# Kernel tuning notes

Measured on AMD Instinct MI355X. Metric: run time of the kernel, lower is better.

Reference implementation:

```python
import jax, jax.numpy as jnp
import numpy as np

B, S, E = 8, 2048, 1024
EPS = 1e-5

def _layernorm(x, w, b):
    mu = jnp.mean(x, axis=-1, keepdims=True)
    var = jnp.mean(jnp.square(x - mu), axis=-1, keepdims=True)
    return (x - mu) * jax.lax.rsqrt(var + EPS) * w + b

def setup_inputs() -> dict:
    key = jax.random.key(0)
    ks = jax.random.split(key, 12)
    x = jax.random.normal(ks[0], (B, S, E), dtype=jnp.float32)
    pad_mask = jax.random.randint(ks[1], (B, 1, S), 0, 2).astype(bool)
    pad_mask = pad_mask.at[:, :, 0].set(False)  # ensure no fully-masked row
    s = 1.0 / np.sqrt(E)
    Wq = jax.random.normal(ks[2], (E, E), jnp.float32) * s
    Wk = jax.random.normal(ks[3], (E, E), jnp.float32) * s
    Wv = jax.random.normal(ks[4], (E, E), jnp.float32) * s
    bq = jnp.zeros((E,), jnp.float32)
    bk = jnp.zeros((E,), jnp.float32)
    bv = jnp.zeros((E,), jnp.float32)
    W1 = jax.random.normal(ks[5], (2 * E, E), jnp.float32) * s
    b1 = jnp.zeros((2 * E,), jnp.float32)
    W2 = jax.random.normal(ks[6], (E, 2 * E), jnp.float32) * (1.0 / np.sqrt(2 * E))
    b2 = jnp.zeros((E,), jnp.float32)
    ln1_w = jnp.ones((E,), jnp.float32); ln1_b = jnp.zeros((E,), jnp.float32)
    ln2_w = jnp.ones((E,), jnp.float32); ln2_b = jnp.zeros((E,), jnp.float32)
    return {"x": x, "pad_mask": pad_mask, "ln1_w": ln1_w, "ln1_b": ln1_b,
            "ln2_w": ln2_w, "ln2_b": ln2_b, "Wq": Wq, "bq": bq, "Wk": Wk,
            "bk": bk, "Wv": Wv, "bv": bv, "W1": W1, "b1": b1, "W2": W2, "b2": b2}

def reference(x, pad_mask, ln1_w, ln1_b, ln2_w, ln2_b, Wq, bq, Wk, bk, Wv, bv, W1, b1, W2, b2):
    scale = jnp.sqrt(jnp.float32(x.shape[-1]))
    normed = _layernorm(x, ln1_w, ln1_b)
    Q = jnp.einsum('bse,de->bsd', normed, Wq) + bq
    K = jnp.einsum('bse,de->bsd', normed, Wk) + bk
    V = jnp.einsum('bse,de->bsd', normed, Wv) + bv
    scores = jnp.einsum('bqd,bkd->bqk', Q, K) / scale  # [B,S,S]
    scores = jnp.where(pad_mask, -jnp.inf, scores)
    attn = jax.nn.softmax(scores, axis=2)  # dropout is identity at inference
    x = x + jnp.einsum('bqk,bkd->bqd', attn, V)
    h = _layernorm(x, ln2_w, ln2_b)
    h = jax.nn.relu(jnp.einsum('bse,fe->bsf', h, W1) + b1)
    x = x + jnp.einsum('bsf,ef->bse', h, W2) + b2
    return x
```

## Files before the change

kernel.cpp:

```cpp
#include <hip/hip_runtime.h>
#include <hip/hip_bf16.h>
#include <cstdint>

#define B_ 8
#define S_ 2048
#define E_ 1024

using u16 = unsigned short;

typedef __bf16 bf16x8 __attribute__((ext_vector_type(8)));
typedef float f32x4 __attribute__((ext_vector_type(4)));

__device__ inline u16 f2bf(float f) {
  uint32_t u = __float_as_uint(f);
  uint32_t r = (u + 0x7fffu + ((u >> 16) & 1u)) >> 16;
  return (u16)r;
}

template<bool HAS_BIAS, bool RELU, bool HAS_RES, bool OUT_BF16, bool SCORES,
         bool GATHER_A, bool RUNTK>
__global__ __launch_bounds__(256, 2) void gemm_nt(
    const u16* __restrict__ A, const u16* __restrict__ B, void* __restrict__ C,
    const float* __restrict__ bias, const float* __restrict__ res,
    int lda, int ldb, int ldc, int K,
    long long strideA, long long strideB, long long strideC,
    const int* __restrict__ cidx, const int* __restrict__ cnt)
{
  __shared__ __attribute__((aligned(16))) u16 lA[2][128 * 64];
  __shared__ __attribute__((aligned(16))) u16 lB[2][128 * 64];

  const int tid  = threadIdx.x;
  const int lane = tid & 63;
  const int wave = tid >> 6;

  const int GM = 8, GN = 4;
  const int nbn = gridDim.x, nbm = gridDim.y, nz = gridDim.z;
  int bm, bn, bz;
  {
    const int total = nbn * nbm * nz;
    const long long lin = blockIdx.x +
        (long long)nbn * (blockIdx.y + (long long)nbm * blockIdx.z);
    if ((nbm % GM) == 0 && (nbn % GN) == 0 && (total % (8 * GM * GN)) == 0) {
      const int xcd = (int)(lin & 7);
      const int loc = (int)(lin >> 3);
      const int sper = GM * GN;
      const int super = (loc / sper) * 8 + xcd;
      const int ins   = loc % sper;
      const int spz = (nbm / GM) * (nbn / GN);
      bz = super / spz;
      const int s2 = super % spz;
      const int sm = s2 % (nbm / GM);
      const int sn = s2 / (nbm / GM);
      bm = sm * GM + (ins % GM);
      bn = sn * GN + (ins / GM);
    } else { bm = blockIdx.y; bn = blockIdx.x; bz = blockIdx.z; }
  }

  int count = 0, cpad = 0;
  if (SCORES || GATHER_A || RUNTK) {
    count = cnt[bz * 2];
    cpad  = cnt[bz * 2 + 1];
    if (GATHER_A && bm * 128 >= cpad) return;
    if (SCORES   && bn * 128 >= cpad) return;
  }
  const int Keff = RUNTK ? cpad : K;
  const int nk = Keff >> 6;

  const u16* Ab = A + (long long)bz * strideA;
  const u16* Bb = B + (long long)bz * strideB;

  const int srow = tid >> 3;
  const int scol = ((tid & 7) ^ (srow & 7)) * 8;
  long long rowA[4], rowB[4];
#pragma unroll
  for (int l = 0; l < 4; ++l) {
    int ra = bm * 128 + srow + l * 32;
    if (GATHER_A) ra = cidx[(long long)bz * S_ + ra];
    rowA[l] = (long long)ra * lda + scol;
    rowB[l] = (long long)(bn * 128 + srow + l * 32) * ldb + scol;
  }
  const int ldsoff = tid * 8;

  const int wr = wave >> 1, wc = wave & 1;
  const int rA = wr * 64 + (lane & 15);
  const int rB = wc * 64 + (lane & 15);
#define LDSP3(P) ((uint32_t)(uintptr_t)(__attribute__((address_space(3))) const void*)(P))
  uint32_t aA0 = LDSP3(&lA[0][0]) +
      2u * (uint32_t)(rA * 64 + (((0 * 4 + (lane >> 4)) ^ (rA & 7)) * 8));
  uint32_t aA1 = LDSP3(&lA[0][0]) +
      2u * (uint32_t)(rA * 64 + (((1 * 4 + (lane >> 4)) ^ (rA & 7)) * 8));
  uint32_t bB0 = LDSP3(&lB[0][0]) +
      2u * (uint32_t)(rB * 64 + (((0 * 4 + (lane >> 4)) ^ (rB & 7)) * 8));
  uint32_t bB1 = LDSP3(&lB[0][0]) +
      2u * (uint32_t)(rB * 64 + (((1 * 4 + (lane >> 4)) ^ (rB & 7)) * 8));
#undef LDSP3

  f32x4 acc[4][4];
#pragma unroll
  for (int mi = 0; mi < 4; ++mi)
#pragma unroll
    for (int ni = 0; ni < 4; ++ni)
      acc[mi][ni] = (f32x4){0.f, 0.f, 0.f, 0.f};

#define STAGE(T) {                                                             \
    const int tt_ = ((T) < nk) ? (T) : (nk - 1);                               \
    _Pragma("unroll") for (int l = 0; l < 4; ++l)                              \
      __builtin_amdgcn_global_load_lds(                                        \
          (const __attribute__((address_space(1))) void*)                      \
              (Ab + rowA[l] + (long long)tt_ * 64),                            \
          (__attribute__((address_space(3))) void*)                            \
              (&lA[(T) & 1][l * 2048 + ldsoff]),                               \
          16, 0, 0);                                                           \
    _Pragma("unroll") for (int l = 0; l < 4; ++l)                              \
      __builtin_amdgcn_global_load_lds(                                        \
          (const __attribute__((address_space(1))) void*)                      \
              (Bb + rowB[l] + (long long)tt_ * 64),                            \
          (__attribute__((address_space(3))) void*)                            \
              (&lB[(T) & 1][l * 2048 + ldsoff]),                               \
          16, 0, 0); }

#define DSR(D, ADDR, OFF) \
    asm volatile("ds_read_b128 %0, %1 offset:" OFF : "=v"(D) : "v"(ADDR))
#define LGKM(NSTR) asm volatile("s_waitcnt lgkmcnt(" NSTR ")" ::: "memory")
#define SCHED0()   __builtin_amdgcn_sched_barrier(0)
#define BAR()      __builtin_amdgcn_s_barrier()

#define MFMA_NI(NI) {                                                          \
    _Pragma("unroll") for (int mi = 0; mi < 4; ++mi)                           \
      _Pragma("unroll") for (int k2 = 0; k2 < 2; ++k2)                         \
        acc[mi][NI] = __builtin_amdgcn_mfma_f32_16x16x32_bf16(                 \
            af[mi][k2], bf[NI][k2], acc[mi][NI], 0, 0, 0); }

  STAGE(0);
  asm volatile("s_waitcnt vmcnt(0)" ::: "memory");
  BAR();

  bf16x8 af[4][2], bf[4][2];
  for (int t = 0; t < nk; ++t) {
    STAGE(t + 1);
    DSR(af[0][0], aA0, "0");     DSR(af[0][1], aA1, "0");
    DSR(af[1][0], aA0, "2048");  DSR(af[1][1], aA1, "2048");
    DSR(af[2][0], aA0, "4096");  DSR(af[2][1], aA1, "4096");
    DSR(af[3][0], aA0, "6144");  DSR(af[3][1], aA1, "6144");
    DSR(bf[0][0], bB0, "0");     DSR(bf[0][1], bB1, "0");
    DSR(bf[1][0], bB0, "2048");  DSR(bf[1][1], bB1, "2048");
    DSR(bf[2][0], bB0, "4096");  DSR(bf[2][1], bB1, "4096");
    DSR(bf[3][0], bB0, "6144");  DSR(bf[3][1], bB1, "6144");
    __builtin_amdgcn_s_setprio(1);
    LGKM("6"); SCHED0(); MFMA_NI(0);
    LGKM("4"); SCHED0(); MFMA_NI(1);
    LGKM("2"); SCHED0(); MFMA_NI(2);
    LGKM("0"); SCHED0(); MFMA_NI(3);
    __builtin_amdgcn_s_setprio(0);
    asm volatile("s_waitcnt vmcnt(0)" ::: "memory");
    BAR();
    const uint32_t d = (t & 1) ? (uint32_t)-16384 : 16384u;
    aA0 += d; aA1 += d; bB0 += d; bB1 += d;
  }

#undef MFMA_NI
#undef DSR
#undef STAGE
#undef BAR
#undef LGKM
#undef SCHED0

  const float* resb = (const float*)C;
  if (HAS_RES) resb = res + (long long)bz * strideC;
  u16*   cb16 = (u16*)C   + (long long)bz * strideC;
  float* cf32 = (float*)C + (long long)bz * strideC;

#pragma unroll
  for (int ni = 0; ni < 4; ++ni) {
    const int gn = bn * 128 + wc * 64 + ni * 16 + (lane & 15);
    const float bvv = HAS_BIAS ? bias[gn] : 0.f;
    const bool cmask = SCORES && (gn >= count);
#pragma unroll
    for (int mi = 0; mi < 4; ++mi) {
#pragma unroll
      for (int r = 0; r < 4; ++r) {
        const int gm = bm * 128 + wr * 64 + mi * 16 + (lane >> 4) * 4 + r;
        const long long idx = (long long)gm * ldc + gn;
        float v = acc[mi][ni][r] + bvv;
        if (SCORES) { v *= 0.03125f; if (cmask) v = -3.0e38f; }
        if (RELU) v = fmaxf(v, 0.f);
        if (HAS_RES) v += resb[idx];
        if (OUT_BF16) cb16[idx] = f2bf(v);
        else          cf32[idx] = v;
      }
    }
  }
}

__global__ __launch_bounds__(256) void layernorm_kernel(
    const float* __restrict__ x, const float* __restrict__ w,
    const float* __restrict__ b, u16* __restrict__ out)
{
  const int row = blockIdx.x;
  const int tid = threadIdx.x;
  const float4 v = ((const float4*)(x + (long long)row * E_))[tid];
  float s  = v.x + v.y + v.z + v.w;
  float s2 = v.x * v.x + v.y * v.y + v.z * v.z + v.w * v.w;
#pragma unroll
  for (int o = 32; o >= 1; o >>= 1) { s += __shfl_xor(s, o); s2 += __shfl_xor(s2, o); }
  __shared__ float rs[4], rs2[4];
  const int wave = tid >> 6, lane = tid & 63;
  if (lane == 0) { rs[wave] = s; rs2[wave] = s2; }
  __syncthreads();
  s  = rs[0] + rs[1] + rs[2] + rs[3];
  s2 = rs2[0] + rs2[1] + rs2[2] + rs2[3];
  const float mu   = s * (1.f / E_);
  const float var  = s2 * (1.f / E_) - mu * mu;
  const float rstd = rsqrtf(var + 1e-5f);
  const float4 wv = ((const float4*)w)[tid];
  const float4 bv = ((const float4*)b)[tid];
  ushort4 o;
  o.x = f2bf((v.x - mu) * rstd * wv.x + bv.x);
  o.y = f2bf((v.y - mu) * rstd * wv.y + bv.y);
  o.z = f2bf((v.z - mu) * rstd * wv.z + bv.z);
  o.w = f2bf((v.w - mu) * rstd * wv.w + bv.w);
  ((ushort4*)(out + (long long)row * E_))[tid] = o;
}

__global__ __launch_bounds__(256) void softmax_bf16_kernel(
    u16* __restrict__ sp, const int* __restrict__ cnt)
{
  const int row = blockIdx.x;
  const int bz  = row >> 11;
  const int tid = threadIdx.x;
  const int cpad = cnt[bz * 2 + 1];
  const bool act = (tid * 8) < cpad;
  u16* pr = sp + (long long)row * S_;

  float v[8];
  if (act) {
    const uint4 raw = ((const uint4*)pr)[tid];
    const uint32_t w[4] = {raw.x, raw.y, raw.z, raw.w};
#pragma unroll
    for (int c = 0; c < 4; ++c) {
      v[2 * c]     = __uint_as_float(w[c] << 16);
      v[2 * c + 1] = __uint_as_float(w[c] & 0xffff0000u);
    }
  } else {
#pragma unroll
    for (int i = 0; i < 8; ++i) v[i] = -3.38e38f;
  }
  float mx = -3.38e38f;
#pragma unroll
  for (int i = 0; i < 8; ++i) mx = fmaxf(mx, v[i]);
#pragma unroll
  for (int o = 32; o >= 1; o >>= 1) mx = fmaxf(mx, __shfl_xor(mx, o));
  __shared__ float red[4];
  const int wave = tid >> 6, lane = tid & 63;
  if (lane == 0) red[wave] = mx;
  __syncthreads();
  mx = fmaxf(fmaxf(red[0], red[1]), fmaxf(red[2], red[3]));

  float s = 0.f;
#pragma unroll
  for (int i = 0; i < 8; ++i) { v[i] = __expf(v[i] - mx); s += v[i]; }
#pragma unroll
  for (int o = 32; o >= 1; o >>= 1) s += __shfl_xor(s, o);
  __syncthreads();
  if (lane == 0) red[wave] = s;
  __syncthreads();
  s = red[0] + red[1] + red[2] + red[3];
  const float inv = 1.f / s;

  if (act) {
    uint4 o4;
    uint32_t* ow = (uint32_t*)&o4;
#pragma unroll
    for (int c = 0; c < 4; ++c) {
      const uint32_t lo = f2bf(v[2 * c] * inv);
      const uint32_t hi = f2bf(v[2 * c + 1] * inv);
      ow[c] = lo | (hi << 16);
    }
    ((uint4*)pr)[tid] = o4;
  }
}

__global__ __launch_bounds__(256) void transpose_kernel(
    const u16* __restrict__ KVc, u16* __restrict__ Vt, const int* __restrict__ cnt)
{
  const int bl = blockIdx.z;
  const int s0 = blockIdx.y * 32;
  if (s0 >= cnt[bl * 2 + 1]) return;
  __shared__ u16 tile[32][33];
  const int e0 = blockIdx.x * 32;
  const int tx = threadIdx.x & 31, ty = threadIdx.x >> 5;
  const u16* src = KVc + ((long long)bl * S_ + s0) * (2 * E_) + E_ + e0;
#pragma unroll
  for (int r = 0; r < 32; r += 8)
    tile[ty + r][tx] = src[(long long)(ty + r) * (2 * E_) + tx];
  __syncthreads();
  u16* dst = Vt + ((long long)bl * E_ + e0) * S_ + s0;
#pragma unroll
  for (int r = 0; r < 32; r += 8)
    dst[(long long)(ty + r) * S_ + tx] = tile[tx][ty + r];
}

__global__ __launch_bounds__(256) void prep_kernel(
    const float* __restrict__ Wq, const float* __restrict__ Wk,
    const float* __restrict__ Wv, const float* __restrict__ W1,
    const float* __restrict__ W2, const float* __restrict__ bk,
    const float* __restrict__ bv,
    u16* __restrict__ Wqb, u16* __restrict__ Wkvb,
    u16* __restrict__ W1b, u16* __restrict__ W2b, float* __restrict__ bkv)
{
  const int N1 = E_ * E_;
  const long long i = (long long)blockIdx.x * 256 + threadIdx.x;
  if (i < N1)               Wqb[i] = f2bf(Wq[i]);
  else if (i < 2LL * N1)    Wkvb[i - N1] = f2bf(Wk[i - N1]);
  else if (i < 3LL * N1)    Wkvb[N1 + (i - 2LL * N1)] = f2bf(Wv[i - 2LL * N1]);
  else if (i < 5LL * N1)    W1b[i - 3LL * N1] = f2bf(W1[i - 3LL * N1]);
  else if (i < 7LL * N1)    W2b[i - 5LL * N1] = f2bf(W2[i - 5LL * N1]);
  else if (i < 7LL * N1 + 2 * E_) {
    const int j = (int)(i - 7LL * N1);
    bkv[j] = (j < E_) ? bk[j] : bv[j - E_];
  }
}

__global__ void detect_kernel(const unsigned char* __restrict__ m, int* __restrict__ flag)
{
  __shared__ int any;
  if (threadIdx.x == 0) any = 0;
  __syncthreads();
  int loc = 0;
  for (int i = threadIdx.x; i < B_ * S_; i += 256)
    if ((i & 3) && m[i]) loc = 1;
  if (loc) atomicOr(&any, 1);
  __syncthreads();
  if (threadIdx.x == 0) *flag = any;
}

__global__ __launch_bounds__(256) void compact_kernel(
    const void* __restrict__ mask, const int* __restrict__ flag,
    int* __restrict__ cidx, int* __restrict__ cnt)
{
  const int b = blockIdx.x;
  const int tid = threadIdx.x, lane = tid & 63, wave = tid >> 6;
  const bool u8m = (*flag != 0);
  const unsigned char* m8 = (const unsigned char*)mask + (long long)b * S_;
  const int* m32 = (const int*)mask + (long long)b * S_;

  int keep[8]; int my = 0;
#pragma unroll
  for (int j = 0; j < 8; ++j) {
    const int s = tid * 8 + j;
    const bool k = u8m ? (m8[s] == 0) : (m32[s] == 0);
    keep[j] = k ? 1 : 0; my += keep[j];
  }
  int pre = my;
#pragma unroll
  for (int o = 1; o < 64; o <<= 1) {
    const int n = __shfl_up(pre, o);
    if (lane >= o) pre += n;
  }
  __shared__ int wsum[4];
  if (lane == 63) wsum[wave] = pre;
  __syncthreads();
  int wbase = 0;
#pragma unroll
  for (int w = 0; w < 4; ++w) if (w < wave) wbase += wsum[w];
  int pos = wbase + pre - my;
  int* cx = cidx + (long long)b * S_;
#pragma unroll
  for (int j = 0; j < 8; ++j)
    if (keep[j]) cx[pos++] = tid * 8 + j;
  const int total = wsum[0] + wsum[1] + wsum[2] + wsum[3];
  const int cpad = (total + 127) & ~127;
  for (int i = total + tid; i < cpad; i += 256) cx[i] = 0;
  if (tid == 0) { cnt[b * 2] = total; cnt[b * 2 + 1] = cpad; }
}

extern "C" void kernel_launch(void* const* d_in, const int* in_sizes, int n_in,
                              void* d_out, int out_size, void* d_ws, size_t ws_size,
                              hipStream_t stream)
{
  const float* x    = (const float*)d_in[0];
  const void*  mask = d_in[1];
  const float* ln1w = (const float*)d_in[2];
  const float* ln1b = (const float*)d_in[3];
  const float* ln2w = (const float*)d_in[4];
  const float* ln2b = (const float*)d_in[5];
  const float* Wq   = (const float*)d_in[6];
  const float* bq   = (const float*)d_in[7];
  const float* Wk   = (const float*)d_in[8];
  const float* bk   = (const float*)d_in[9];
  const float* Wv   = (const float*)d_in[10];
  const float* bv   = (const float*)d_in[11];
  const float* W1   = (const float*)d_in[12];
  const float* b1   = (const float*)d_in[13];
  const float* W2   = (const float*)d_in[14];
  const float* b2   = (const float*)d_in[15];

  const size_t MB = 1024ull * 1024ull;
  char* p = (char*)d_ws;
  int* flag    = (int*)p;   p += 256;
  int* cnt     = (int*)p;   p += 256;
  int* cidx    = (int*)p;   p += (size_t)B_ * S_ * 4;
  u16* Wqb     = (u16*)p;   p += (size_t)E_ * E_ * 2;
  u16* Wkvb    = (u16*)p;   p += (size_t)2 * E_ * E_ * 2;
  u16* W1b     = (u16*)p;   p += (size_t)2 * E_ * E_ * 2;
  u16* W2b     = (u16*)p;   p += (size_t)2 * E_ * E_ * 2;
  float* bkv   = (float*)p; p += 2 * E_ * 4;
  u16* normedb = (u16*)p;   p += (size_t)B_ * S_ * E_ * 2;
  char* chunk  = p;
  const size_t used  = (size_t)(p - (char*)d_ws);
  const size_t avail = (ws_size > used) ? (ws_size - used) : 0;

  int bc = 1;
  for (int c = 8; c >= 1; c >>= 1)
    if (avail >= 24 * MB * (size_t)c) { bc = c; break; }

  float* out = (float*)d_out;
  dim3 blk(256);
  dim3 blkg(256);

  detect_kernel<<<1, 256, 0, stream>>>((const unsigned char*)mask, flag);
  compact_kernel<<<B_, blk, 0, stream>>>(mask, flag, cidx, cnt);
  {
    const long long tot = 7LL * E_ * E_ + 2 * E_;
    prep_kernel<<<(int)((tot + 255) / 256), blk, 0, stream>>>(
        Wq, Wk, Wv, W1, W2, bk, bv, Wqb, Wkvb, W1b, W2b, bkv);
  }

  layernorm_kernel<<<B_ * S_, blk, 0, stream>>>(x, ln1w, ln1b, normedb);

  for (int b0 = 0; b0 < B_; b0 += bc) {
    u16* Qc  = (u16*)chunk;
    u16* KVc = Qc + (size_t)bc * S_ * E_;
    u16* Vt  = KVc + (size_t)bc * S_ * 2 * E_;
    u16* Pc  = Vt + (size_t)bc * E_ * S_;
    const int* cntb  = cnt + b0 * 2;
    const int* cidxb = cidx + (size_t)b0 * S_;

    gemm_nt<true, false, false, true, false, false, false>
        <<<dim3(E_ / 128, bc * S_ / 128, 1), blkg, 0, stream>>>(
        normedb + (size_t)b0 * S_ * E_, Wqb, Qc, bq, nullptr,
        E_, E_, E_, E_, 0, 0, 0, nullptr, nullptr);

    gemm_nt<true, false, false, true, false, true, false>
        <<<dim3(2 * E_ / 128, S_ / 128, bc), blkg, 0, stream>>>(
        normedb + (size_t)b0 * S_ * E_, Wkvb, KVc, bkv, nullptr,
        E_, E_, 2 * E_, E_,
        (long long)S_ * E_, 0, (long long)S_ * 2 * E_, cidxb, cntb);

    transpose_kernel<<<dim3(E_ / 32, S_ / 32, bc), blk, 0, stream>>>(KVc, Vt, cntb);

    gemm_nt<false, false, false, true, true, false, false>
        <<<dim3(S_ / 128, S_ / 128, bc), blkg, 0, stream>>>(
        Qc, KVc, Pc, nullptr, nullptr,
        E_, 2 * E_, S_, E_,
        (long long)S_ * E_, (long long)S_ * 2 * E_, (long long)S_ * S_,
        nullptr, cntb);

    softmax_bf16_kernel<<<bc * S_, blk, 0, stream>>>(Pc, cntb);

    gemm_nt<false, false, true, false, false, false, true>
        <<<dim3(E_ / 128, S_ / 128, bc), blkg, 0, stream>>>(
        Pc, Vt, out + (size_t)b0 * S_ * E_, nullptr,
        x + (size_t)b0 * S_ * E_, S_, S_, E_, S_,
        (long long)S_ * S_, (long long)E_ * S_, (long long)S_ * E_,
        nullptr, cntb);
  }

  layernorm_kernel<<<B_ * S_, blk, 0, stream>>>(out, ln2w, ln2b, normedb);

  size_t mr_sz = avail / ((size_t)2 * E_ * 2);
  int mr = (int)((mr_sz > 16384) ? 16384 : mr_sz);
  mr &= ~127;
  if (mr < 128) mr = 128;
  u16* hb = (u16*)chunk;
  for (int m0 = 0; m0 < B_ * S_; m0 += mr) {
    const int mm = (B_ * S_ - m0 < mr) ? (B_ * S_ - m0) : mr;
    gemm_nt<true, true, false, true, false, false, false>
        <<<dim3((2 * E_) / 128, mm / 128, 1), blkg, 0, stream>>>(
        normedb + (size_t)m0 * E_, W1b, hb, b1, nullptr,
        E_, E_, 2 * E_, E_, 0, 0, 0, nullptr, nullptr);
    gemm_nt<true, false, true, false, false, false, false>
        <<<dim3(E_ / 128, mm / 128, 1), blkg, 0, stream>>>(
        hb, W2b, out + (size_t)m0 * E_, b2, out + (size_t)m0 * E_,
        2 * E_, 2 * E_, E_, 2 * E_, 0, 0, 0, nullptr, nullptr);
  }
}
```

Baseline: 652.3 us.

## Shrink GEMM K-tile to 32 and drop LDS double buffering for higher occupancy

The GEMM kernel moves from a double-buffered 64-wide K tile to a single-buffered 32-wide K tile, cutting LDS use from 64KB to 16KB per block and raising the launch-bounds occupancy hint from 2 to 4 blocks per CU. The LDS swizzle is adapted to the narrower rows. Because there is now only one buffer, the global-to-LDS copy for the next tile is issued only after the current tile's MFMAs and a barrier, then waited on, so load and compute no longer overlap inside a block. The bet is that more resident blocks hide that latency, in exchange for twice as many iterations and barriers.

```diff
diff --git a/kernel.cpp b/kernel.cpp
--- a/kernel.cpp
+++ b/kernel.cpp
@@ -19,15 +19,15 @@
 
 template<bool HAS_BIAS, bool RELU, bool HAS_RES, bool OUT_BF16, bool SCORES,
          bool GATHER_A, bool RUNTK>
-__global__ __launch_bounds__(256, 2) void gemm_nt(
+__global__ __launch_bounds__(256, 4) void gemm_nt(
     const u16* __restrict__ A, const u16* __restrict__ B, void* __restrict__ C,
     const float* __restrict__ bias, const float* __restrict__ res,
     int lda, int ldb, int ldc, int K,
     long long strideA, long long strideB, long long strideC,
     const int* __restrict__ cidx, const int* __restrict__ cnt)
 {
-  __shared__ __attribute__((aligned(16))) u16 lA[2][128 * 64];
-  __shared__ __attribute__((aligned(16))) u16 lB[2][128 * 64];
+  __shared__ __attribute__((aligned(16))) u16 lA[128 * 32];
+  __shared__ __attribute__((aligned(16))) u16 lB[128 * 32];
 
   const int tid  = threadIdx.x;
   const int lane = tid & 63;
@@ -64,20 +64,20 @@
     if (SCORES   && bn * 128 >= cpad) return;
   }
   const int Keff = RUNTK ? cpad : K;
-  const int nk = Keff >> 6;
+  const int nk = Keff >> 5;
 
   const u16* Ab = A + (long long)bz * strideA;
   const u16* Bb = B + (long long)bz * strideB;
 
-  const int srow = tid >> 3;
-  const int scol = ((tid & 7) ^ (srow & 7)) * 8;
-  long long rowA[4], rowB[4];
-#pragma unroll
-  for (int l = 0; l < 4; ++l) {
-    int ra = bm * 128 + srow + l * 32;
+  const int srow = tid >> 2;
+  const int scol = ((tid & 3) ^ (srow & 3) ^ ((srow >> 2) & 1)) * 8;
+  long long rowA[2], rowB[2];
+#pragma unroll
+  for (int l = 0; l < 2; ++l) {
+    int ra = bm * 128 + srow + l * 64;
     if (GATHER_A) ra = cidx[(long long)bz * S_ + ra];
     rowA[l] = (long long)ra * lda + scol;
-    rowB[l] = (long long)(bn * 128 + srow + l * 32) * ldb + scol;
+    rowB[l] = (long long)(bn * 128 + srow + l * 64) * ldb + scol;
   }
   const int ldsoff = tid * 8;
 
@@ -85,14 +85,10 @@
   const int rA = wr * 64 + (lane & 15);
   const int rB = wc * 64 + (lane & 15);
 #define LDSP3(P) ((uint32_t)(uintptr_t)(__attribute__((address_space(3))) const void*)(P))
-  uint32_t aA0 = LDSP3(&lA[0][0]) +
-      2u * (uint32_t)(rA * 64 + (((0 * 4 + (lane >> 4)) ^ (rA & 7)) * 8));
-  uint32_t aA1 = LDSP3(&lA[0][0]) +
-      2u * (uint32_t)(rA * 64 + (((1 * 4 + (lane >> 4)) ^ (rA & 7)) * 8));
-  uint32_t bB0 = LDSP3(&lB[0][0]) +
-      2u * (uint32_t)(rB * 64 + (((0 * 4 + (lane >> 4)) ^ (rB & 7)) * 8));
-  uint32_t bB1 = LDSP3(&lB[0][0]) +
-      2u * (uint32_t)(rB * 64 + (((1 * 4 + (lane >> 4)) ^ (rB & 7)) * 8));
+  const uint32_t aA = LDSP3(&lA[0]) +
+      2u * (uint32_t)(rA * 32 + (((lane >> 4) ^ (rA & 3) ^ ((rA >> 2) & 1)) * 8));
+  const uint32_t bB = LDSP3(&lB[0]) +
+      2u * (uint32_t)(rB * 32 + (((lane >> 4) ^ (rB & 3) ^ ((rB >> 2) & 1)) * 8));
 #undef LDSP3
 
   f32x4 acc[4][4];
@@ -104,19 +100,19 @@
 
 #define STAGE(T) {                                                             \
     const int tt_ = ((T) < nk) ? (T) : (nk - 1);                               \
-    _Pragma("unroll") for (int l = 0; l < 4; ++l)                              \
+    _Pragma("unroll") for (int l = 0; l < 2; ++l)                              \
       __builtin_amdgcn_global_load_lds(                                        \
           (const __attribute__((address_space(1))) void*)                      \
-              (Ab + rowA[l] + (long long)tt_ * 64),                            \
+              (Ab + rowA[l] + (long long)tt_ * 32),                            \
           (__attribute__((address_space(3))) void*)                            \
-              (&lA[(T) & 1][l * 2048 + ldsoff]),                               \
+              (&lA[l * 2048 + ldsoff]),                                        \
           16, 0, 0);                                                           \
-    _Pragma("unroll") for (int l = 0; l < 4; ++l)                              \
+    _Pragma("unroll") for (int l = 0; l < 2; ++l)                              \
       __builtin_amdgcn_global_load_lds(                                        \
           (const __attribute__((address_space(1))) void*)                      \
-              (Bb + rowB[l] + (long long)tt_ * 64),                            \
+              (Bb + rowB[l] + (long long)tt_ * 32),                            \
           (__attribute__((address_space(3))) void*)                            \
-              (&lB[(T) & 1][l * 2048 + ldsoff]),                               \
+              (&lB[l * 2048 + ldsoff]),                                        \
           16, 0, 0); }
 
 #define DSR(D, ADDR, OFF) \
@@ -127,35 +123,29 @@
 
 #define MFMA_NI(NI) {                                                          \
     _Pragma("unroll") for (int mi = 0; mi < 4; ++mi)                           \
-      _Pragma("unroll") for (int k2 = 0; k2 < 2; ++k2)                         \
         acc[mi][NI] = __builtin_amdgcn_mfma_f32_16x16x32_bf16(                 \
-            af[mi][k2], bf[NI][k2], acc[mi][NI], 0, 0, 0); }
+            af[mi], bf[NI], acc[mi][NI], 0, 0, 0); }
 
   STAGE(0);
   asm volatile("s_waitcnt vmcnt(0)" ::: "memory");
   BAR();
 
-  bf16x8 af[4][2], bf[4][2];
+  bf16x8 af[4], bf[4];
   for (int t = 0; t < nk; ++t) {
-    STAGE(t + 1);
-    DSR(af[0][0], aA0, "0");     DSR(af[0][1], aA1, "0");
-    DSR(af[1][0], aA0, "2048");  DSR(af[1][1], aA1, "2048");
-    DSR(af[2][0], aA0, "4096");  DSR(af[2][1], aA1, "4096");
-    DSR(af[3][0], aA0, "6144");  DSR(af[3][1], aA1, "6144");
-    DSR(bf[0][0], bB0, "0");     DSR(bf[0][1], bB1, "0");
-    DSR(bf[1][0], bB0, "2048");  DSR(bf[1][1], bB1, "2048");
-    DSR(bf[2][0], bB0, "4096");  DSR(bf[2][1], bB1, "4096");
-    DSR(bf[3][0], bB0, "6144");  DSR(bf[3][1], bB1, "6144");
+    DSR(af[0], aA, "0");     DSR(af[1], aA, "1024");
+    DSR(af[2], aA, "2048");  DSR(af[3], aA, "3072");
+    DSR(bf[0], bB, "0");     DSR(bf[1], bB, "1024");
+    DSR(bf[2], bB, "2048");  DSR(bf[3], bB, "3072");
     __builtin_amdgcn_s_setprio(1);
-    LGKM("6"); SCHED0(); MFMA_NI(0);
-    LGKM("4"); SCHED0(); MFMA_NI(1);
-    LGKM("2"); SCHED0(); MFMA_NI(2);
+    LGKM("3"); SCHED0(); MFMA_NI(0);
+    LGKM("2"); SCHED0(); MFMA_NI(1);
+    LGKM("1"); SCHED0(); MFMA_NI(2);
     LGKM("0"); SCHED0(); MFMA_NI(3);
     __builtin_amdgcn_s_setprio(0);
+    BAR();
+    STAGE(t + 1);
     asm volatile("s_waitcnt vmcnt(0)" ::: "memory");
     BAR();
-    const uint32_t d = (t & 1) ? (uint32_t)-16384 : 16384u;
-    aA0 += d; aA1 += d; bB0 += d; bB1 += d;
   }
 
 #undef MFMA_NI
```

Measured after the change: 745.6 us. 14.3% more time.
